# Kernel tuning notes

Hardware: AMD Instinct MI355X
Metric: run time of the kernel (lower is better)

Reference implementation:

```python
import jax, jax.numpy as jnp
import numpy as np

N_HEADS = 16
HEAD_DIM = 64
WINDOW = 128
GLOBAL = 64


def setup_inputs() -> dict:
    key = jax.random.key(0)
    ks = jax.random.split(key, 5)
    B, T, D = 2, 8192, 1024
    s = 0.02
    return {
        "x": jax.random.normal(ks[0], (B, T, D), dtype=jnp.float32),
        "Wq": jax.random.normal(ks[1], (D, D), dtype=jnp.float32) * s,
        "Wk": jax.random.normal(ks[2], (D, D), dtype=jnp.float32) * s,
        "Wv": jax.random.normal(ks[3], (D, D), dtype=jnp.float32) * s,
        "Wo": jax.random.normal(ks[4], (D, D), dtype=jnp.float32) * s,
    }


def reference(x, Wq, Wk, Wv, Wo):
    B, T, D = x.shape
    h, hd, w = N_HEADS, HEAD_DIM, WINDOW
    g = min(GLOBAL, T)
    nw = T // w  # T chosen as a multiple of window_size
    scale = hd ** -0.5

    def proj(W):
        # nn.Linear: y = x @ W.T ; then (B,T,h,hd) -> (B,h,T,hd)
        return (x @ W.T).reshape(B, T, h, hd).transpose(0, 2, 1, 3)

    q = proj(Wq)
    k = proj(Wk)
    v = proj(Wv)

    # Chunk into non-overlapping local windows: (B,h,nw,w,hd)
    qw = q.reshape(B, h, nw, w, hd)
    kw = k.reshape(B, h, nw, w, hd)
    vw = v.reshape(B, h, nw, w, hd)
    kg = k[:, :, :g, :]  # global prefix keys (B,h,g,hd)
    vg = v[:, :, :g, :]

    # Scores against [global ++ local] keys (faithful: global prefix is
    # concatenated for every window, including windows that overlap it).
    s_g = jnp.einsum("bhnqd,bhgd->bhnqg", qw, kg) * scale  # (B,h,nw,w,g)
    s_l = jnp.einsum("bhnqd,bhnkd->bhnqk", qw, kw) * scale  # (B,h,nw,w,w)
    attn = jax.nn.softmax(jnp.concatenate([s_g, s_l], axis=-1), axis=-1)

    out = (
        jnp.einsum("bhnqg,bhgd->bhnqd", attn[..., :g], vg)
        + jnp.einsum("bhnqk,bhnkd->bhnqd", attn[..., g:], vw)
    )
    out = out.reshape(B, h, T, hd).transpose(0, 2, 1, 3).reshape(B, T, D)
    return out @ Wo.T
```

## Files before the change

kernel.cpp:

```cpp
#include <hip/hip_runtime.h>

typedef unsigned short u16;
typedef __attribute__((ext_vector_type(8))) short short8;
typedef __attribute__((ext_vector_type(4))) float f32x4;
typedef __attribute__((ext_vector_type(4))) float floatx4;
typedef __attribute__((ext_vector_type(4))) unsigned short ushort4v;
typedef __attribute__((ext_vector_type(8))) unsigned short ushort8v;

#define MFMA(a, b, c) __builtin_amdgcn_mfma_f32_16x16x32_bf16(a, b, c, 0, 0, 0)

__device__ __forceinline__ u16 f2bf(float f) {
    unsigned u = __float_as_uint(f);
    u += 0x7fffu + ((u >> 16) & 1u);
    return (u16)(u >> 16);
}

__device__ __forceinline__ void async16(const void* g, void* l) {
    __builtin_amdgcn_global_load_lds(
        (const __attribute__((address_space(1))) void*)g,
        (__attribute__((address_space(3))) void*)l, 16, 0, 0);
}

__global__ void cvt_bf16(const float* __restrict__ s, u16* __restrict__ d, int n4) {
    int i = blockIdx.x * blockDim.x + threadIdx.x;
    int stride = gridDim.x * blockDim.x;
    for (; i < n4; i += stride) {
        floatx4 v = ((const floatx4*)s)[i];
        ushort4v o;
        o[0] = f2bf(v[0]); o[1] = f2bf(v[1]); o[2] = f2bf(v[2]); o[3] = f2bf(v[3]);
        ((ushort4v*)d)[i] = o;
    }
}

__global__ void cvt4_bf16(const float* __restrict__ s0, const float* __restrict__ s1,
                          const float* __restrict__ s2, const float* __restrict__ s3,
                          u16* __restrict__ d, int n4) {
    const float* s = blockIdx.y == 0 ? s0 : (blockIdx.y == 1 ? s1 : (blockIdx.y == 2 ? s2 : s3));
    u16* dd = d + (size_t)blockIdx.y * n4 * 4;
    int i = blockIdx.x * blockDim.x + threadIdx.x;
    int stride = gridDim.x * blockDim.x;
    for (; i < n4; i += stride) {
        floatx4 v = ((const floatx4*)s)[i];
        ushort4v o;
        o[0] = f2bf(v[0]); o[1] = f2bf(v[1]); o[2] = f2bf(v[2]); o[3] = f2bf(v[3]);
        ((ushort4v*)dd)[i] = o;
    }
}

template <bool BF16_OUT>
__global__ __launch_bounds__(256) void gemm_nt(
    const u16* __restrict__ A, const u16* __restrict__ B0,
    const u16* __restrict__ B1, const u16* __restrict__ B2,
    void* __restrict__ Cv, int M, int N, int K)
{
    __shared__ u16 As[128 * 64];
    __shared__ u16 Bs[128 * 64];
    const int tid = threadIdx.x;
    const int wave = tid >> 6, lane = tid & 63;
    const int quad = lane >> 4, tl = lane & 15;
    const int m0 = blockIdx.x * 128, n0 = blockIdx.y * 128;
    const int wm = wave >> 1, wn = wave & 1;
    const u16* Bm = blockIdx.z == 0 ? B0 : (blockIdx.z == 1 ? B1 : B2);
    const size_t coff = (size_t)blockIdx.z * M * N;

    f32x4 acc[4][4];
#pragma unroll
    for (int i = 0; i < 4; i++)
#pragma unroll
        for (int j = 0; j < 4; j++) acc[i][j] = (f32x4)(0.0f);

    const int srow = tid >> 3, sslot = tid & 7;

    for (int k0 = 0; k0 < K; k0 += 64) {
#pragma unroll
        for (int i = 0; i < 4; i++) {
            int row = i * 32 + srow;
            int g = sslot ^ (row & 7);
            int ldsbase = (i * 256 + wave * 64) * 8;
            async16(A  + (size_t)(m0 + row) * K + k0 + g * 8, (u16*)As + ldsbase);
            async16(Bm + (size_t)(n0 + row) * K + k0 + g * 8, (u16*)Bs + ldsbase);
        }
        __syncthreads();
#pragma unroll
        for (int h = 0; h < 2; h++) {
            short8 af[4], bg[4];
            const int rs = (((h * 4 + quad) ^ (tl & 7)) * 8);
#pragma unroll
            for (int t = 0; t < 4; t++) {
                af[t] = *(const short8*)&As[(wm * 64 + t * 16 + tl) * 64 + rs];
                bg[t] = *(const short8*)&Bs[(wn * 64 + t * 16 + tl) * 64 + rs];
            }
#pragma unroll
            for (int mt = 0; mt < 4; mt++)
#pragma unroll
                for (int nt = 0; nt < 4; nt++)
                    acc[mt][nt] = MFMA(af[mt], bg[nt], acc[mt][nt]);
        }
        __syncthreads();
    }

#pragma unroll
    for (int mt = 0; mt < 4; mt++)
#pragma unroll
        for (int nt = 0; nt < 4; nt++)
#pragma unroll
            for (int r = 0; r < 4; r++) {
                int row = m0 + wm * 64 + mt * 16 + quad * 4 + r;
                int col = n0 + wn * 64 + nt * 16 + tl;
                if constexpr (BF16_OUT)
                    ((u16*)Cv)[coff + (size_t)row * N + col] = f2bf(acc[mt][nt][r]);
                else
                    ((float*)Cv)[coff + (size_t)row * N + col] = acc[mt][nt][r];
            }
}

__global__ __launch_bounds__(256) void attn_win(
    const u16* __restrict__ qkv, u16* __restrict__ outb)
{
    constexpr int T = 8192, D = 1024, HD = 64, G = 64, WIN = 128;
    constexpr int MTOT = 2 * T;
    __shared__ u16 Vt[64 * 200];
    __shared__ u16 KP[12800];

    const int blk = blockIdx.x;
    const int half = blk & 1;
    const int nwin = (blk >> 1) & 63;
    const int h = (blk >> 7) & 15;
    const int b = blk >> 11;
    const int tid = threadIdx.x;
    const int wave = tid >> 6, lane = tid & 63;
    const int quad = lane >> 4, tl = lane & 15;
    const int win0 = nwin * WIN;
    const int q0 = win0 + half * 64;
    const size_t brow = (size_t)b * T;
    const u16* qb = qkv;
    const u16* kb = qkv + (size_t)MTOT * D;
    const u16* vb = qkv + (size_t)2 * MTOT * D;

#pragma unroll
    for (int i = 0; i < 6; i++) {
        int ch = i * 256 + tid;
        int row = ch >> 3, c = ch & 7;
        int tok = row < G ? row : win0 + (row - G);
        async16(vb + (brow + tok) * D + h * HD + c * 8,
                (u16*)KP + (i * 256 + wave * 64) * 8);
    }

    short8 bq[2];
    {
        int tok = q0 + wave * 16 + tl;
        const u16* qrow = qb + (brow + tok) * D + h * HD;
        bq[0] = *(const short8*)(qrow + quad * 8);
        bq[1] = *(const short8*)(qrow + 32 + quad * 8);
    }

    __syncthreads();

    {
        const int d = tid & 63;
#pragma unroll
        for (int i = 0; i < 6; i++) {
            int c = i * 4 + wave;
            ushort8v v;
#pragma unroll
            for (int j = 0; j < 8; j++) v[j] = KP[(c * 8 + j) * 64 + d];
            *(ushort8v*)&Vt[d * 200 + c * 8] = v;
        }
    }

    __syncthreads();

#pragma unroll
    for (int i = 0; i < 6; i++) {
        int ch = i * 256 + tid;
        int row = ch >> 3, slot = ch & 7;
        int g = slot ^ (row & 7);
        int tok = row < G ? row : win0 + (row - G);
        async16(kb + (brow + tok) * D + h * HD + g * 8,
                (u16*)KP + (i * 256 + wave * 64) * 8);
    }

    __syncthreads();

    f32x4 s[12];
#pragma unroll
    for (int kt = 0; kt < 12; kt++) s[kt] = (f32x4)(0.0f);
#pragma unroll
    for (int kt = 0; kt < 12; kt++) {
        int row = kt * 16 + tl;
        int s0 = quad ^ (tl & 7);
        int s1 = (4 + quad) ^ (tl & 7);
        short8 a0 = *(const short8*)&KP[row * 64 + s0 * 8];
        short8 a1 = *(const short8*)&KP[row * 64 + s1 * 8];
        s[kt] = MFMA(a0, bq[0], s[kt]);
        s[kt] = MFMA(a1, bq[1], s[kt]);
    }

    const float c1 = 0.125f * 1.4426950408889634f;
    float mx = -1e30f;
#pragma unroll
    for (int kt = 0; kt < 12; kt++)
#pragma unroll
        for (int r = 0; r < 4; r++) mx = fmaxf(mx, s[kt][r]);
    mx = fmaxf(mx, __shfl_xor(mx, 16, 64));
    mx = fmaxf(mx, __shfl_xor(mx, 32, 64));
    float sum = 0.f;
#pragma unroll
    for (int kt = 0; kt < 12; kt++)
#pragma unroll
        for (int r = 0; r < 4; r++) {
            float e = exp2f((s[kt][r] - mx) * c1);
            s[kt][r] = e;
            sum += e;
        }
    sum += __shfl_xor(sum, 16, 64);
    sum += __shfl_xor(sum, 32, 64);
    float inv = 1.f / sum;

    __syncthreads();

    u16* Pl = (u16*)KP;
    {
        int lq = wave * 16 + tl;
#pragma unroll
        for (int kt = 0; kt < 12; kt++) {
            ushort4v p;
#pragma unroll
            for (int r = 0; r < 4; r++) p[r] = f2bf(s[kt][r] * inv);
            *(ushort4v*)&Pl[lq * 200 + kt * 16 + quad * 4] = p;
        }
    }
    __syncthreads();

    f32x4 o[4];
#pragma unroll
    for (int dt = 0; dt < 4; dt++) o[dt] = (f32x4)(0.0f);
#pragma unroll
    for (int ks = 0; ks < 6; ks++) {
        short8 pa = *(const short8*)&Pl[(wave * 16 + tl) * 200 + ks * 32 + quad * 8];
#pragma unroll
        for (int dt = 0; dt < 4; dt++) {
            short8 vv = *(const short8*)&Vt[(dt * 16 + tl) * 200 + ks * 32 + quad * 8];
            o[dt] = MFMA(pa, vv, o[dt]);
        }
    }

#pragma unroll
    for (int dt = 0; dt < 4; dt++)
#pragma unroll
        for (int r = 0; r < 4; r++) {
            int qq = q0 + wave * 16 + quad * 4 + r;
            int dim = dt * 16 + tl;
            outb[(brow + qq) * D + h * HD + dim] = f2bf(o[dt][r]);
        }
}

extern "C" void kernel_launch(void* const* d_in, const int* in_sizes, int n_in,
                              void* d_out, int out_size, void* d_ws, size_t ws_size,
                              hipStream_t stream)
{
    const float* x  = (const float*)d_in[0];
    const float* Wq = (const float*)d_in[1];
    const float* Wk = (const float*)d_in[2];
    const float* Wv = (const float*)d_in[3];
    const float* Wo = (const float*)d_in[4];

    const int M = 16384, D = 1024;
    u16* xb  = (u16*)d_ws;
    u16* wqb = xb  + (size_t)M * D;
    u16* wob = wqb + (size_t)3 * D * D;
    u16* qkv = wob + (size_t)D * D;
    u16* att = qkv + (size_t)3 * M * D;

    cvt_bf16<<<2048, 256, 0, stream>>>(x, xb, M * D / 4);
    cvt4_bf16<<<dim3(64, 4), 256, 0, stream>>>(Wq, Wk, Wv, Wo, wqb, D * D / 4);

    gemm_nt<true ><<<dim3(M / 128, D / 128, 3), 256, 0, stream>>>(
        xb, wqb, wqb + (size_t)D * D, wqb + (size_t)2 * D * D, qkv, M, D, D);
    attn_win<<<dim3(4096), 256, 0, stream>>>(qkv, att);
    gemm_nt<false><<<dim3(M / 128, D / 128, 1), 256, 0, stream>>>(
        att, wob, wob, wob, d_out, M, D, D);
}
```

Baseline: 339.4 us.

## Process whole window per block and pass P to PV MFMA via lane shuffles

Each block now handles all 128 queries of a window (two 16-row query tiles per wave) instead of half a window, so the K/V global loads and the V transpose into LDS are shared by twice as many queries and the grid is halved. The softmax probabilities are packed to bf16 in registers and rearranged into the MFMA A-operand layout with cross-lane shuffles, which removes the LDS round trip and its two barriers. In exchange there are more shuffle instructions, higher register pressure, and fewer blocks to fill the GPU.

```diff
diff --git a/kernel.cpp b/kernel.cpp
--- a/kernel.cpp
+++ b/kernel.cpp
@@ -6,6 +6,7 @@
 typedef __attribute__((ext_vector_type(4))) float floatx4;
 typedef __attribute__((ext_vector_type(4))) unsigned short ushort4v;
 typedef __attribute__((ext_vector_type(8))) unsigned short ushort8v;
+typedef __attribute__((ext_vector_type(4))) unsigned int uint4v;
 
 #define MFMA(a, b, c) __builtin_amdgcn_mfma_f32_16x16x32_bf16(a, b, c, 0, 0, 0)
 
@@ -120,18 +121,16 @@
     constexpr int T = 8192, D = 1024, HD = 64, G = 64, WIN = 128;
     constexpr int MTOT = 2 * T;
     __shared__ u16 Vt[64 * 200];
-    __shared__ u16 KP[12800];
+    __shared__ u16 KP[192 * 64];
 
     const int blk = blockIdx.x;
-    const int half = blk & 1;
-    const int nwin = (blk >> 1) & 63;
-    const int h = (blk >> 7) & 15;
-    const int b = blk >> 11;
+    const int nwin = blk & 63;
+    const int h = (blk >> 6) & 15;
+    const int b = blk >> 10;
     const int tid = threadIdx.x;
     const int wave = tid >> 6, lane = tid & 63;
     const int quad = lane >> 4, tl = lane & 15;
     const int win0 = nwin * WIN;
-    const int q0 = win0 + half * 64;
     const size_t brow = (size_t)b * T;
     const u16* qb = qkv;
     const u16* kb = qkv + (size_t)MTOT * D;
@@ -146,18 +145,19 @@
                 (u16*)KP + (i * 256 + wave * 64) * 8);
     }
 
-    short8 bq[2];
+    short8 bq[2][2];
+#pragma unroll
+    for (int qt = 0; qt < 2; qt++) {
+        int tok = win0 + (wave * 2 + qt) * 16 + tl;
+        const u16* qrow = qb + (brow + tok) * D + h * HD;
+        bq[qt][0] = *(const short8*)(qrow + quad * 8);
+        bq[qt][1] = *(const short8*)(qrow + 32 + quad * 8);
+    }
+
+    __syncthreads();
+
     {
-        int tok = q0 + wave * 16 + tl;
-        const u16* qrow = qb + (brow + tok) * D + h * HD;
-        bq[0] = *(const short8*)(qrow + quad * 8);
-        bq[1] = *(const short8*)(qrow + 32 + quad * 8);
-    }
-
-    __syncthreads();
-
-    {
-        const int d = tid & 63;
+        const int d = lane;
 #pragma unroll
         for (int i = 0; i < 6; i++) {
             int c = i * 4 + wave;
@@ -182,77 +182,88 @@
 
     __syncthreads();
 
-    f32x4 s[12];
-#pragma unroll
-    for (int kt = 0; kt < 12; kt++) s[kt] = (f32x4)(0.0f);
-#pragma unroll
-    for (int kt = 0; kt < 12; kt++) {
-        int row = kt * 16 + tl;
-        int s0 = quad ^ (tl & 7);
-        int s1 = (4 + quad) ^ (tl & 7);
-        short8 a0 = *(const short8*)&KP[row * 64 + s0 * 8];
-        short8 a1 = *(const short8*)&KP[row * 64 + s1 * 8];
-        s[kt] = MFMA(a0, bq[0], s[kt]);
-        s[kt] = MFMA(a1, bq[1], s[kt]);
-    }
-
     const float c1 = 0.125f * 1.4426950408889634f;
-    float mx = -1e30f;
-#pragma unroll
-    for (int kt = 0; kt < 12; kt++)
-#pragma unroll
-        for (int r = 0; r < 4; r++) mx = fmaxf(mx, s[kt][r]);
-    mx = fmaxf(mx, __shfl_xor(mx, 16, 64));
-    mx = fmaxf(mx, __shfl_xor(mx, 32, 64));
-    float sum = 0.f;
-#pragma unroll
-    for (int kt = 0; kt < 12; kt++)
-#pragma unroll
-        for (int r = 0; r < 4; r++) {
-            float e = exp2f((s[kt][r] - mx) * c1);
-            s[kt][r] = e;
-            sum += e;
-        }
-    sum += __shfl_xor(sum, 16, 64);
-    sum += __shfl_xor(sum, 32, 64);
-    float inv = 1.f / sum;
-
-    __syncthreads();
-
-    u16* Pl = (u16*)KP;
-    {
-        int lq = wave * 16 + tl;
+    const int s0sl = quad ^ (tl & 7);
+    const int s1sl = (4 + quad) ^ (tl & 7);
+    const int tsel = quad >> 1;
+    const int src0 = tl + 32 * (quad & 1);
+
+#pragma unroll
+    for (int qt = 0; qt < 2; qt++) {
+        f32x4 s[12];
+#pragma unroll
+        for (int kt = 0; kt < 12; kt++) s[kt] = (f32x4)(0.0f);
 #pragma unroll
         for (int kt = 0; kt < 12; kt++) {
-            ushort4v p;
-#pragma unroll
-            for (int r = 0; r < 4; r++) p[r] = f2bf(s[kt][r] * inv);
-            *(ushort4v*)&Pl[lq * 200 + kt * 16 + quad * 4] = p;
-        }
-    }
-    __syncthreads();
-
-    f32x4 o[4];
-#pragma unroll
-    for (int dt = 0; dt < 4; dt++) o[dt] = (f32x4)(0.0f);
-#pragma unroll
-    for (int ks = 0; ks < 6; ks++) {
-        short8 pa = *(const short8*)&Pl[(wave * 16 + tl) * 200 + ks * 32 + quad * 8];
-#pragma unroll
-        for (int dt = 0; dt < 4; dt++) {
-            short8 vv = *(const short8*)&Vt[(dt * 16 + tl) * 200 + ks * 32 + quad * 8];
-            o[dt] = MFMA(pa, vv, o[dt]);
-        }
-    }
-
-#pragma unroll
-    for (int dt = 0; dt < 4; dt++)
-#pragma unroll
-        for (int r = 0; r < 4; r++) {
-            int qq = q0 + wave * 16 + quad * 4 + r;
-            int dim = dt * 16 + tl;
-            outb[(brow + qq) * D + h * HD + dim] = f2bf(o[dt][r]);
-        }
+            int row = kt * 16 + tl;
+            short8 a0 = *(const short8*)&KP[row * 64 + s0sl * 8];
+            short8 a1 = *(const short8*)&KP[row * 64 + s1sl * 8];
+            s[kt] = MFMA(a0, bq[qt][0], s[kt]);
+            s[kt] = MFMA(a1, bq[qt][1], s[kt]);
+        }
+
+        float mx = -1e30f;
+#pragma unroll
+        for (int kt = 0; kt < 12; kt++)
+#pragma unroll
+            for (int r = 0; r < 4; r++) mx = fmaxf(mx, s[kt][r]);
+        mx = fmaxf(mx, __shfl_xor(mx, 16, 64));
+        mx = fmaxf(mx, __shfl_xor(mx, 32, 64));
+        float sum = 0.f;
+#pragma unroll
+        for (int kt = 0; kt < 12; kt++)
+#pragma unroll
+            for (int r = 0; r < 4; r++) {
+                float e = exp2f((s[kt][r] - mx) * c1);
+                s[kt][r] = e;
+                sum += e;
+            }
+        sum += __shfl_xor(sum, 16, 64);
+        sum += __shfl_xor(sum, 32, 64);
+        float inv = 1.f / sum;
+
+        unsigned pk0[12], pk1[12];
+#pragma unroll
+        for (int kt = 0; kt < 12; kt++) {
+            pk0[kt] = (unsigned)f2bf(s[kt][0] * inv) | ((unsigned)f2bf(s[kt][1] * inv) << 16);
+            pk1[kt] = (unsigned)f2bf(s[kt][2] * inv) | ((unsigned)f2bf(s[kt][3] * inv) << 16);
+        }
+
+        f32x4 o[4];
+#pragma unroll
+        for (int dt = 0; dt < 4; dt++) o[dt] = (f32x4)(0.0f);
+#pragma unroll
+        for (int c = 0; c < 6; c++) {
+            unsigned f0a = (unsigned)__shfl((int)pk0[2 * c],     src0,      64);
+            unsigned f0b = (unsigned)__shfl((int)pk0[2 * c + 1], src0,      64);
+            unsigned f1a = (unsigned)__shfl((int)pk1[2 * c],     src0,      64);
+            unsigned f1b = (unsigned)__shfl((int)pk1[2 * c + 1], src0,      64);
+            unsigned f2a = (unsigned)__shfl((int)pk0[2 * c],     src0 + 16, 64);
+            unsigned f2b = (unsigned)__shfl((int)pk0[2 * c + 1], src0 + 16, 64);
+            unsigned f3a = (unsigned)__shfl((int)pk1[2 * c],     src0 + 16, 64);
+            unsigned f3b = (unsigned)__shfl((int)pk1[2 * c + 1], src0 + 16, 64);
+            uint4v fr;
+            fr[0] = tsel ? f0b : f0a;
+            fr[1] = tsel ? f1b : f1a;
+            fr[2] = tsel ? f2b : f2a;
+            fr[3] = tsel ? f3b : f3a;
+            short8 pa = __builtin_bit_cast(short8, fr);
+#pragma unroll
+            for (int dt = 0; dt < 4; dt++) {
+                short8 vv = *(const short8*)&Vt[(dt * 16 + tl) * 200 + c * 32 + quad * 8];
+                o[dt] = MFMA(pa, vv, o[dt]);
+            }
+        }
+
+#pragma unroll
+        for (int dt = 0; dt < 4; dt++)
+#pragma unroll
+            for (int r = 0; r < 4; r++) {
+                int qq = win0 + (wave * 2 + qt) * 16 + quad * 4 + r;
+                int dim = dt * 16 + tl;
+                outb[(brow + qq) * D + h * HD + dim] = f2bf(o[dt][r]);
+            }
+    }
 }
 
 extern "C" void kernel_launch(void* const* d_in, const int* in_sizes, int n_in,
@@ -277,7 +288,7 @@
 
     gemm_nt<true ><<<dim3(M / 128, D / 128, 3), 256, 0, stream>>>(
         xb, wqb, wqb + (size_t)D * D, wqb + (size_t)2 * D * D, qkv, M, D, D);
-    attn_win<<<dim3(4096), 256, 0, stream>>>(qkv, att);
+    attn_win<<<dim3(2048), 256, 0, stream>>>(qkv, att);
     gemm_nt<false><<<dim3(M / 128, D / 128, 1), 256, 0, stream>>>(
         att, wob, wob, wob, d_out, M, D, D);
 }
```

Measured after the change: 350.1 us. +3.2%, slower.
